# Kernel tuning notes

Hardware: AMD Instinct MI355X
Metric: run time of the kernel (lower is better)

## Reference

```python
import jax, jax.numpy as jnp
import numpy as np

B, N, T, CIN, HID, EMB, K = 32, 256, 13, 2, 64, 10, 2


def setup_inputs() -> dict:
    key = jax.random.key(0)
    ks = jax.random.split(key, 24)
    r = lambda i, shape, s=1.0: jax.random.normal(ks[i], shape, jnp.float32) * s
    return {
        "times": jnp.arange(T, dtype=jnp.float32),
        # natural cubic spline coefficients: (B, N, T-1, CIN)
        "coeff_a": r(0, (B, N, T - 1, CIN)),
        "coeff_b": r(1, (B, N, T - 1, CIN), 0.1),
        "coeff_two_c": r(2, (B, N, T - 1, CIN), 0.1),
        "coeff_three_d": r(3, (B, N, T - 1, CIN), 0.1),
        # initial_h / initial_z linear layers (input -> hidden)
        "W_h": r(4, (CIN, HID), 0.5), "b_h": r(5, (HID,), 0.1),
        "W_z": r(6, (CIN, HID), 0.5), "b_z": r(7, (HID,), 0.1),
        # func_f (FinalTanh_f): linear_in, one hidden linear, linear_out -> hidden*input
        "Wf_in": r(8, (HID, HID), 0.1), "bf_in": r(9, (HID,), 0.05),
        "Wf_hid": r(10, (HID, HID), 0.1), "bf_hid": r(11, (HID,), 0.05),
        "Wf_out": r(12, (HID, HID * CIN), 0.1), "bf_out": r(13, (HID * CIN,), 0.05),
        # func_g (VectorField_g, g_type='agc')
        "Wg_in": r(14, (HID, HID), 0.1), "bg_in": r(15, (HID,), 0.05),
        "Eg": r(16, (N, EMB)),
        "W_pool": r(17, (EMB, K, HID, HID), 0.1),
        "b_pool": r(18, (EMB, HID), 0.1),
        "Wg_out": r(19, (HID, HID * CIN), 0.1), "bg_out": r(20, (HID * CIN,), 0.05),
    }


def reference(times, coeff_a, coeff_b, coeff_two_c, coeff_three_d,
              W_h, b_h, W_z, b_z,
              Wf_in, bf_in, Wf_hid, bf_hid, Wf_out, bf_out,
              Wg_in, bg_in, Eg, W_pool, b_pool, Wg_out, bg_out):
    maxidx = coeff_b.shape[-2] - 1

    def dX_dt(t):  # NaturalCubicSpline.derivative
        idx = jnp.clip(jnp.searchsorted(times, t, side='right') - 1, 0, maxidx)
        frac = t - times[idx]
        b = coeff_b[..., idx, :]
        c = coeff_two_c[..., idx, :]
        d = coeff_three_d[..., idx, :]
        return b + (c + d * frac) * frac  # (B, N, CIN)

    # adaptive graph conv (agc) static pieces, cheb_k = 2
    A = jax.nn.softmax(jax.nn.relu(Eg @ Eg.T), axis=1)          # (N, N)
    supports = jnp.stack([jnp.eye(N, dtype=A.dtype), A])        # (K, N, N)
    Wn = jnp.einsum('nd,dkio->nkio', Eg, W_pool)                # (N, K, HID, HID)
    bn = Eg @ b_pool                                            # (N, HID)

    def func_f(h):  # FinalTanh_f: MLP -> (B, N, HID, CIN) field
        x = jax.nn.relu(h @ Wf_in + bf_in)
        x = jax.nn.relu(x @ Wf_hid + bf_hid)
        x = (x @ Wf_out + bf_out).reshape(*x.shape[:-1], HID, CIN)
        return jnp.tanh(x)

    def func_g(z):  # VectorField_g with agc
        x = jax.nn.relu(z @ Wg_in + bg_in)                       # (B, N, HID)
        x_g = jnp.einsum('knm,bmc->bnkc', supports, x)           # (B, N, K, HID)
        x = jnp.einsum('bnki,nkio->bno', x_g, Wn) + bn           # (B, N, HID)
        x = (x @ Wg_out + bg_out).reshape(*x.shape[:-1], HID, CIN)
        return jnp.tanh(x)

    def vf(t, h, z):  # VectorField_g_dev of cdeint_gde_dev
        dX = dX_dt(t)                                            # (B, N, CIN)
        f = func_f(h)
        g = func_g(z)
        dh = jnp.einsum('bnhi,bni->bnh', f, dX)
        dz = jnp.einsum('bnhi,bni->bnh', g * f, dX)
        return dh, dz

    # spline.evaluate(times[0]) == coeff_a[..., 0, :] (frac = 0)
    x0 = coeff_a[..., 0, :]
    h0 = x0 @ W_h + b_h
    z0 = x0 @ W_z + b_z

    third = jnp.float32(1.0 / 3.0)

    def step(carry, ts):  # torchdiffeq 'rk4' (3/8 rule), one step per interval
        h, z = carry
        t0, t1 = ts
        dt = t1 - t0
        k1h, k1z = vf(t0, h, z)
        k2h, k2z = vf(t0 + dt * third, h + dt * third * k1h, z + dt * third * k1z)
        k3h, k3z = vf(t0 + dt * 2 * third, h + dt * (k2h - third * k1h), z + dt * (k2z - third * k1z))
        k4h, k4z = vf(t1, h + dt * (k1h - k2h + k3h), z + dt * (k1z - k2z + k3z))
        h = h + dt * 0.125 * (k1h + 3.0 * (k2h + k3h) + k4h)
        z = z + dt * 0.125 * (k1z + 3.0 * (k2z + k3z) + k4z)
        return (h, z), z

    ts = jnp.stack([times[:-1], times[1:]], axis=1)              # (T-1, 2)
    (_, _), z_seq = jax.lax.scan(step, (h0, z0), ts)
    z_t = jnp.concatenate([z0[None], z_seq], axis=0)             # (T, B, N, HID)
    return jnp.transpose(z_t, (1, 2, 0, 3))                      # (B, N, T, HID)
```

## Files before the change

kernel.cpp:

```cpp
#include <hip/hip_runtime.h>

typedef unsigned short ushort_t;
typedef unsigned int uint_t;
typedef float f4v __attribute__((ext_vector_type(4)));

#define CW_OFF  0
#define A_OFF   524288
#define BN_OFF  786432
#define WN_OFF  851968
#define XB_OFF  5046272
#define H_OFF   7143424
#define Z_OFF   9240576
#define K1H_OFF 11337728
#define K1Z_OFF 13434880
#define K2H_OFF 15532032
#define K2Z_OFF 17629184
#define UH_OFF  19726336

#define F_X0     0
#define F_WH     16384
#define F_BH     16512
#define F_WZ     16576
#define F_BZ     16704
#define F_WFIN   16768
#define F_BFIN   20864
#define F_WFHID  20928
#define F_BFHID  25024
#define F_WFOUT  25088
#define F_BFOUT  33280
#define F_WGIN   33408
#define F_BGIN   37504
#define F_WGOUT  37568
#define F_BGOUT  45760
#define F_EG     45888
#define F_WPOOL  48448
#define F_BPOOL  130368

__device__ __forceinline__ float bfl(uint_t u){ union{uint_t i; float f;} c; c.i = u<<16; return c.f; }
__device__ __forceinline__ float bfh(uint_t u){ union{uint_t i; float f;} c; c.i = u & 0xffff0000u; return c.f; }
__device__ __forceinline__ float bf1(ushort_t u){ union{uint_t i; float f;} c; c.i = ((uint_t)u)<<16; return c.f; }
__device__ __forceinline__ uint_t f2bf(float x){
  uint_t u = __float_as_uint(x);
  uint_t r = u + 0x7fffu + ((u >> 16) & 1u);
  return r >> 16;
}
__device__ __forceinline__ float fast_tanh(float x){
  float e = __expf(2.0f*x);
  return 1.0f - 2.0f/(e+1.0f);
}
__device__ __forceinline__ bool inputs_are_f32(const void* times){
  return ((const uint_t*)times)[0] != 0x3F800000u;
}
__device__ __forceinline__ void ntst4(float* p, float a, float b, float c, float d){
  f4v v; v[0]=a; v[1]=b; v[2]=c; v[3]=d;
  __builtin_nontemporal_store(v, (f4v*)p);
}

__device__ __forceinline__ void dotf_4(const float* act, const float* W, int o0, float acc[4]) {
  const float4* a4 = (const float4*)act;
  #pragma unroll
  for (int i4 = 0; i4 < 16; ++i4) {
    float4 av4 = a4[i4];
    float av[4] = {av4.x, av4.y, av4.z, av4.w};
    #pragma unroll
    for (int ii = 0; ii < 4; ++ii) {
      float4 w = *(const float4*)(W + (i4*4+ii)*64 + o0);
      acc[0] += av[ii]*w.x; acc[1] += av[ii]*w.y;
      acc[2] += av[ii]*w.z; acc[3] += av[ii]*w.w;
    }
  }
}

__device__ __forceinline__ void dotf_8(const float* act, const float* W, int co0, float acc[8]) {
  const float4* a4 = (const float4*)act;
  #pragma unroll
  for (int i4 = 0; i4 < 16; ++i4) {
    float4 av4 = a4[i4];
    float av[4] = {av4.x, av4.y, av4.z, av4.w};
    #pragma unroll
    for (int ii = 0; ii < 4; ++ii) {
      const float* wp = W + (i4*4+ii)*128 + co0;
      float4 w0 = *(const float4*)(wp);
      float4 w1 = *(const float4*)(wp + 4);
      float a = av[ii];
      acc[0] += a*w0.x; acc[1] += a*w0.y; acc[2] += a*w0.z; acc[3] += a*w0.w;
      acc[4] += a*w1.x; acc[5] += a*w1.y; acc[6] += a*w1.z; acc[7] += a*w1.w;
    }
  }
}

__device__ __forceinline__ void cvt_copy(float* dst, const void* src, int cnt, bool f32in){
  if (f32in) {
    const float* s = (const float*)src;
    for (int i = threadIdx.x; i < cnt; i += 256) dst[i] = s[i];
  } else {
    const ushort_t* s = (const ushort_t*)src;
    for (int i = threadIdx.x; i < cnt; i += 256) dst[i] = bf1(s[i]);
  }
}

__global__ __launch_bounds__(256) void k_conv(
    const void* times, const void* ca,
    const void* W_h, const void* b_h, const void* W_z, const void* b_z,
    const void* Wf_in, const void* bf_in, const void* Wf_hid, const void* bf_hid,
    const void* Wf_out, const void* bf_out, const void* Wg_in, const void* bg_in,
    const void* Wg_out, const void* bg_out, const void* Eg, const void* W_pool,
    const void* b_pool, char* __restrict__ wsb)
{
  const bool f32in = inputs_are_f32(times);
  float* F = (float*)(wsb + CW_OFF);
  const int bid = blockIdx.x;
  if (bid < 4) {
    const int base = bid * 4096;
    if (f32in) {
      const float* s = (const float*)ca;
      for (int i = threadIdx.x; i < 4096; i += 256) {
        int g = base + i;
        F[F_X0 + g] = s[(g >> 1)*24 + (g & 1)];
      }
    } else {
      const ushort_t* s = (const ushort_t*)ca;
      for (int i = threadIdx.x; i < 4096; i += 256) {
        int g = base + i;
        F[F_X0 + g] = bf1(s[(g >> 1)*24 + (g & 1)]);
      }
    }
    return;
  }
  if (bid < 20) {
    const int off = (bid - 4) * 5120;
    const void* srcp = f32in ? (const void*)((const float*)W_pool + off)
                             : (const void*)((const ushort_t*)W_pool + off);
    cvt_copy(F + F_WPOOL + off, srcp, 5120, f32in);
    return;
  }
  const void* src = nullptr; int dst = 0, cnt = 0;
  switch (bid) {
    case 20: src = W_h;    dst = F_WH;    cnt = 128;  break;
    case 21: src = b_h;    dst = F_BH;    cnt = 64;   break;
    case 22: src = W_z;    dst = F_WZ;    cnt = 128;  break;
    case 23: src = b_z;    dst = F_BZ;    cnt = 64;   break;
    case 24: src = Wf_in;  dst = F_WFIN;  cnt = 4096; break;
    case 25: src = bf_in;  dst = F_BFIN;  cnt = 64;   break;
    case 26: src = Wf_hid; dst = F_WFHID; cnt = 4096; break;
    case 27: src = bf_hid; dst = F_BFHID; cnt = 64;   break;
    case 28: src = Wf_out; dst = F_WFOUT; cnt = 8192; break;
    case 29: src = bf_out; dst = F_BFOUT; cnt = 128;  break;
    case 30: src = Wg_in;  dst = F_WGIN;  cnt = 4096; break;
    case 31: src = bg_in;  dst = F_BGIN;  cnt = 64;   break;
    case 32: src = Wg_out; dst = F_WGOUT; cnt = 8192; break;
    case 33: src = bg_out; dst = F_BGOUT; cnt = 128;  break;
    case 34: src = Eg;     dst = F_EG;    cnt = 2560; break;
    default: src = b_pool; dst = F_BPOOL; cnt = 640;  break;
  }
  cvt_copy(F + dst, src, cnt, f32in);
}

__global__ __launch_bounds__(256) void k_A(char* __restrict__ wsb) {
  const float* F = (const float*)(wsb + CW_OFF);
  float* Aw = (float*)(wsb + A_OFF);
  float* bn = (float*)(wsb + BN_OFF);
  const int nrow = blockIdx.x;
  const int m = threadIdx.x;
  float eg_n[10];
  #pragma unroll
  for (int d = 0; d < 10; ++d) eg_n[d] = F[F_EG + nrow*10 + d];
  float dot = 0.f;
  #pragma unroll
  for (int d = 0; d < 10; ++d) dot += eg_n[d] * F[F_EG + m*10 + d];
  float v = fmaxf(dot, 0.f);
  __shared__ float red[256];
  red[m] = v; __syncthreads();
  for (int off = 128; off > 0; off >>= 1) {
    if (m < off) red[m] = fmaxf(red[m], red[m+off]);
    __syncthreads();
  }
  float vmax = red[0]; __syncthreads();
  float e = __expf(v - vmax);
  red[m] = e; __syncthreads();
  for (int off = 128; off > 0; off >>= 1) {
    if (m < off) red[m] += red[m+off];
    __syncthreads();
  }
  float ssum = red[0];
  Aw[nrow*256 + m] = e / ssum;
  if (m < 64) {
    float acc = 0.f;
    #pragma unroll
    for (int d = 0; d < 10; ++d) acc += eg_n[d] * F[F_BPOOL + d*64 + m];
    bn[nrow*64 + m] = acc;
  }
}

__global__ __launch_bounds__(256) void k_Wn(char* __restrict__ wsb) {
  const float* F = (const float*)(wsb + CW_OFF);
  ushort_t* Wn = (ushort_t*)(wsb + WN_OFF);
  int idx = blockIdx.x*256 + threadIdx.x;
  int o = idx & 63;
  int i = (idx >> 6) & 63;
  int k = (idx >> 12) & 1;
  int n = idx >> 13;
  float acc = 0.f;
  #pragma unroll
  for (int d = 0; d < 10; ++d)
    acc += F[F_EG + n*10 + d] * F[F_WPOOL + ((d*2 + k)*64 + i)*64 + o];
  Wn[idx] = (ushort_t)f2bf(acc);
}

__global__ __launch_bounds__(512) void k_init2(char* __restrict__ wsb, float* __restrict__ out) {
  const float* F = (const float*)(wsb + CW_OFF);
  float* H = (float*)(wsb + H_OFF);
  float* Z = (float*)(wsb + Z_OFF);
  ushort_t* X0 = (ushort_t*)(wsb + XB_OFF);

  const int tid = threadIdx.x;
  const int lr  = tid >> 4;
  const int o0  = (tid & 15) * 4;
  const int row = blockIdx.x * 32 + lr;

  __shared__ __align__(16) float sIn[32][68];

  float a0 = F[F_X0 + row*2 + 0];
  float a1 = F[F_X0 + row*2 + 1];
  float h[4], z[4];
  #pragma unroll
  for (int j = 0; j < 4; ++j) {
    h[j] = a0*F[F_WH + o0+j] + a1*F[F_WH + 64+o0+j] + F[F_BH + o0+j];
    z[j] = a0*F[F_WZ + o0+j] + a1*F[F_WZ + 64+o0+j] + F[F_BZ + o0+j];
  }
  *(float4*)(H + row*64 + o0) = make_float4(h[0],h[1],h[2],h[3]);
  *(float4*)(Z + row*64 + o0) = make_float4(z[0],z[1],z[2],z[3]);
  ntst4(out + (row*13)*64 + o0, z[0],z[1],z[2],z[3]);

  *(float4*)&sIn[lr][o0] = make_float4(z[0],z[1],z[2],z[3]);
  __syncthreads();
  float xr[4];
  { float4 bv = *(const float4*)(F + F_BGIN + o0);
    xr[0]=bv.x; xr[1]=bv.y; xr[2]=bv.z; xr[3]=bv.w; }
  dotf_4(&sIn[lr][0], F + F_WGIN, o0, xr);
  #pragma unroll
  for (int j=0;j<4;++j) xr[j] = fmaxf(xr[j], 0.f);
  { uint2 pk;
    pk.x = f2bf(xr[0]) | (f2bf(xr[1]) << 16);
    pk.y = f2bf(xr[2]) | (f2bf(xr[3]) << 16);
    *(uint2*)(X0 + row*64 + o0) = pk; }
}

__global__ __launch_bounds__(512) void k_stage(
    const void* __restrict__ times,
    const void* __restrict__ cbv, const void* __restrict__ ccv, const void* __restrict__ cdv,
    char* __restrict__ wsb, float* __restrict__ out, int vfc)
{
  const float* F  = (const float*)(wsb + CW_OFF);
  const float* Aw = (const float*)(wsb + A_OFF);
  const float* bn = (const float*)(wsb + BN_OFF);
  const ushort_t* Wn = (const ushort_t*)(wsb + WN_OFF);
  ushort_t* XB = (ushort_t*)(wsb + XB_OFF);
  float* H   = (float*)(wsb + H_OFF);
  float* Z   = (float*)(wsb + Z_OFF);
  float* K1h = (float*)(wsb + K1H_OFF);
  float* K1z = (float*)(wsb + K1Z_OFF);
  float* K2h = (float*)(wsb + K2H_OFF);
  float* K2z = (float*)(wsb + K2Z_OFF);
  float* UH  = (float*)(wsb + UH_OFF);
  const bool f32in = inputs_are_f32(times);

  const int s  = vfc >> 2;
  const int st = vfc & 3;
  const ushort_t* Xc = XB + (vfc & 1) * 524288;
  ushort_t*       Xn = XB + ((vfc + 1) & 1) * 524288;

  const int tid = threadIdx.x;
  const int lr  = tid >> 4;
  const int o0  = (tid & 15) * 4;
  const int co0 = o0 * 2;
  const int bb  = blockIdx.x >> 3;
  const int nr  = blockIdx.x & 7;
  const int n   = nr * 32 + lr;
  const int row = bb * 256 + n;

  __shared__ __align__(16) float sIn[32][68];
  __shared__ __align__(16) float sT [32][68];
  __shared__ __align__(16) float sX [32][68];
  __shared__ __align__(16) float xs [128][68];

  { uint2 w = *(const uint2*)(Xc + row*64 + o0);
    *(float4*)&sX[lr][o0] = make_float4(bfl(w.x), bfh(w.x), bfl(w.y), bfh(w.y)); }

  float y[4] = {0.f,0.f,0.f,0.f};
  const float* Arow = Aw + n*256;
  #pragma unroll 1
  for (int half = 0; half < 2; ++half) {
    __syncthreads();
    #pragma unroll
    for (int q = tid; q < 2048; q += 512) {
      int r = q >> 4, c4 = q & 15;
      uint2 w = *(const uint2*)(Xc + (bb*256 + half*128 + r)*64 + c4*4);
      *(float4*)&xs[r][c4*4] = make_float4(bfl(w.x), bfh(w.x), bfl(w.y), bfh(w.y));
    }
    __syncthreads();
    #pragma unroll 4
    for (int m4 = 0; m4 < 32; ++m4) {
      float4 av = *(const float4*)(Arow + half*128 + m4*4);
      float am[4] = {av.x, av.y, av.z, av.w};
      #pragma unroll
      for (int mm = 0; mm < 4; ++mm) {
        float4 xv = *(const float4*)&xs[m4*4+mm][o0];
        y[0] += am[mm]*xv.x; y[1] += am[mm]*xv.y;
        y[2] += am[mm]*xv.z; y[3] += am[mm]*xv.w;
      }
    }
  }

  __syncthreads();
  *(float4*)&sT[lr][o0] = make_float4(y[0],y[1],y[2],y[3]);
  __syncthreads();
  float og[4];
  { float4 bv = *(const float4*)(bn + n*64 + o0); og[0]=bv.x; og[1]=bv.y; og[2]=bv.z; og[3]=bv.w; }
  const ushort_t* W0 = Wn + n*8192;
  #pragma unroll
  for (int i4 = 0; i4 < 16; ++i4) {
    float4 xa = *(const float4*)&sX[lr][i4*4];
    float4 ya = *(const float4*)&sT[lr][i4*4];
    float xav[4]={xa.x,xa.y,xa.z,xa.w};
    float yav[4]={ya.x,ya.y,ya.z,ya.w};
    #pragma unroll
    for (int ii = 0; ii < 4; ++ii) {
      int i = i4*4 + ii;
      uint2 w0 = *(const uint2*)(W0 + i*64 + o0);
      uint2 w1 = *(const uint2*)(W0 + 4096 + i*64 + o0);
      og[0] += xav[ii]*bfl(w0.x) + yav[ii]*bfl(w1.x);
      og[1] += xav[ii]*bfh(w0.x) + yav[ii]*bfh(w1.x);
      og[2] += xav[ii]*bfl(w0.y) + yav[ii]*bfl(w1.y);
      og[3] += xav[ii]*bfh(w0.y) + yav[ii]*bfh(w1.y);
    }
  }
  *(float4*)&sIn[lr][o0] = make_float4(og[0],og[1],og[2],og[3]);
  __syncthreads();
  float go[8];
  { float4 b0 = *(const float4*)(F + F_BGOUT + co0);
    float4 b1 = *(const float4*)(F + F_BGOUT + co0 + 4);
    go[0]=b0.x; go[1]=b0.y; go[2]=b0.z; go[3]=b0.w;
    go[4]=b1.x; go[5]=b1.y; go[6]=b1.z; go[7]=b1.w; }
  dotf_8(&sIn[lr][0], F + F_WGOUT, co0, go);
  float g0[4], g1[4];
  #pragma unroll
  for (int j=0;j<4;++j){ g0[j]=fast_tanh(go[2*j]); g1[j]=fast_tanh(go[2*j+1]); }

  __syncthreads();
  { const float* UHsrc = (st == 0) ? H : UH;
    float4 uv = *(const float4*)(UHsrc + row*64 + o0);
    *(float4*)&sIn[lr][o0] = uv; }
  __syncthreads();
  float a1v[4];
  { float4 bv = *(const float4*)(F + F_BFIN + o0);
    a1v[0]=bv.x; a1v[1]=bv.y; a1v[2]=bv.z; a1v[3]=bv.w; }
  dotf_4(&sIn[lr][0], F + F_WFIN, o0, a1v);
  #pragma unroll
  for (int j=0;j<4;++j) a1v[j] = fmaxf(a1v[j], 0.f);
  *(float4*)&sT[lr][o0] = make_float4(a1v[0],a1v[1],a1v[2],a1v[3]);
  __syncthreads();
  float a2v[4];
  { float4 bv = *(const float4*)(F + F_BFHID + o0);
    a2v[0]=bv.x; a2v[1]=bv.y; a2v[2]=bv.z; a2v[3]=bv.w; }
  dotf_4(&sT[lr][0], F + F_WFHID, o0, a2v);
  #pragma unroll
  for (int j=0;j<4;++j) a2v[j] = fmaxf(a2v[j], 0.f);
  *(float4*)&sIn[lr][o0] = make_float4(a2v[0],a2v[1],a2v[2],a2v[3]);
  __syncthreads();
  float fo[8];
  { float4 b0 = *(const float4*)(F + F_BFOUT + co0);
    float4 b1 = *(const float4*)(F + F_BFOUT + co0 + 4);
    fo[0]=b0.x; fo[1]=b0.y; fo[2]=b0.z; fo[3]=b0.w;
    fo[4]=b1.x; fo[5]=b1.y; fo[6]=b1.z; fo[7]=b1.w; }
  dotf_8(&sIn[lr][0], F + F_WFOUT, co0, fo);
  float f0[4], f1[4];
  #pragma unroll
  for (int j=0;j<4;++j){ f0[j]=fast_tanh(fo[2*j]); f1[j]=fast_tanh(fo[2*j+1]); }

  int sidx; float frac;
  if (st == 0)      { sidx = s; frac = 0.f; }
  else if (st == 1) { sidx = s; frac = 0.33333334f; }
  else if (st == 2) { sidx = s; frac = 0.66666669f; }
  else              { sidx = (s < 11) ? s+1 : 11; frac = (s < 11) ? 0.f : 1.f; }
  float dX0, dX1;
  if (f32in) {
    float2 vb = *(const float2*)((const float*)cbv + (row*12 + sidx)*2);
    float2 vc = *(const float2*)((const float*)ccv + (row*12 + sidx)*2);
    float2 vd = *(const float2*)((const float*)cdv + (row*12 + sidx)*2);
    dX0 = vb.x + (vc.x + vd.x*frac)*frac;
    dX1 = vb.y + (vc.y + vd.y*frac)*frac;
  } else {
    uint_t vb = *(const uint_t*)((const ushort_t*)cbv + (row*12 + sidx)*2);
    uint_t vc = *(const uint_t*)((const ushort_t*)ccv + (row*12 + sidx)*2);
    uint_t vd = *(const uint_t*)((const ushort_t*)cdv + (row*12 + sidx)*2);
    dX0 = bfl(vb) + (bfl(vc) + bfl(vd)*frac)*frac;
    dX1 = bfh(vb) + (bfh(vc) + bfh(vd)*frac)*frac;
  }

  float dh[4], dz[4];
  #pragma unroll
  for (int j=0;j<4;++j){
    dh[j] = f0[j]*dX0 + f1[j]*dX1;
    dz[j] = g0[j]*f0[j]*dX0 + g1[j]*f1[j]*dX1;
  }

  float uh_n[4], uz_n[4];
  float4 hv = *(const float4*)(H + row*64 + o0);
  float4 zv = *(const float4*)(Z + row*64 + o0);
  float h[4] = {hv.x,hv.y,hv.z,hv.w};
  float z[4] = {zv.x,zv.y,zv.z,zv.w};

  if (st == 0) {
    *(float4*)(K1h + row*64 + o0) = make_float4(dh[0],dh[1],dh[2],dh[3]);
    *(float4*)(K1z + row*64 + o0) = make_float4(dz[0],dz[1],dz[2],dz[3]);
    #pragma unroll
    for (int j=0;j<4;++j){ uh_n[j]=h[j]+dh[j]*(1.f/3.f); uz_n[j]=z[j]+dz[j]*(1.f/3.f); }
  } else if (st == 1) {
    float4 k1hv = *(const float4*)(K1h + row*64 + o0);
    float4 k1zv = *(const float4*)(K1z + row*64 + o0);
    float k1hl[4]={k1hv.x,k1hv.y,k1hv.z,k1hv.w};
    float k1zl[4]={k1zv.x,k1zv.y,k1zv.z,k1zv.w};
    float Qh[4],Qz[4],Ph[4],Pz[4];
    #pragma unroll
    for (int j=0;j<4;++j){
      Qh[j]=k1hl[j]+3.f*dh[j]; Qz[j]=k1zl[j]+3.f*dz[j];
      Ph[j]=k1hl[j]-dh[j];     Pz[j]=k1zl[j]-dz[j];
      uh_n[j]=h[j]+dh[j]-k1hl[j]*(1.f/3.f);
      uz_n[j]=z[j]+dz[j]-k1zl[j]*(1.f/3.f);
    }
    *(float4*)(K1h + row*64 + o0) = make_float4(Qh[0],Qh[1],Qh[2],Qh[3]);
    *(float4*)(K1z + row*64 + o0) = make_float4(Qz[0],Qz[1],Qz[2],Qz[3]);
    *(float4*)(K2h + row*64 + o0) = make_float4(Ph[0],Ph[1],Ph[2],Ph[3]);
    *(float4*)(K2z + row*64 + o0) = make_float4(Pz[0],Pz[1],Pz[2],Pz[3]);
  } else if (st == 2) {
    float4 Qhv = *(const float4*)(K1h + row*64 + o0);
    float4 Qzv = *(const float4*)(K1z + row*64 + o0);
    float4 Phv = *(const float4*)(K2h + row*64 + o0);
    float4 Pzv = *(const float4*)(K2z + row*64 + o0);
    float Qh[4]={Qhv.x,Qhv.y,Qhv.z,Qhv.w}, Qz[4]={Qzv.x,Qzv.y,Qzv.z,Qzv.w};
    float Ph[4]={Phv.x,Phv.y,Phv.z,Phv.w}, Pz[4]={Pzv.x,Pzv.y,Pzv.z,Pzv.w};
    float Ah[4],Az[4];
    #pragma unroll
    for (int j=0;j<4;++j){
      Ah[j]=Qh[j]+3.f*dh[j]; Az[j]=Qz[j]+3.f*dz[j];
      uh_n[j]=h[j]+Ph[j]+dh[j];
      uz_n[j]=z[j]+Pz[j]+dz[j];
    }
    *(float4*)(K1h + row*64 + o0) = make_float4(Ah[0],Ah[1],Ah[2],Ah[3]);
    *(float4*)(K1z + row*64 + o0) = make_float4(Az[0],Az[1],Az[2],Az[3]);
  } else {
    float4 Ahv = *(const float4*)(K1h + row*64 + o0);
    float4 Azv = *(const float4*)(K1z + row*64 + o0);
    #pragma unroll
    for (int j=0;j<4;++j){
      float hn = h[j] + 0.125f*(((const float*)&Ahv)[j] + dh[j]);
      float zn = z[j] + 0.125f*(((const float*)&Azv)[j] + dz[j]);
      uh_n[j]=hn; uz_n[j]=zn;
    }
    *(float4*)(H + row*64 + o0) = make_float4(uh_n[0],uh_n[1],uh_n[2],uh_n[3]);
    *(float4*)(Z + row*64 + o0) = make_float4(uz_n[0],uz_n[1],uz_n[2],uz_n[3]);
    ntst4(out + (row*13 + s + 1)*64 + o0, uz_n[0],uz_n[1],uz_n[2],uz_n[3]);
  }

  if (vfc < 47) {
    *(float4*)(UH + row*64 + o0) = make_float4(uh_n[0],uh_n[1],uh_n[2],uh_n[3]);
    __syncthreads();
    *(float4*)&sIn[lr][o0] = make_float4(uz_n[0],uz_n[1],uz_n[2],uz_n[3]);
    __syncthreads();
    float xr[4];
    { float4 bv = *(const float4*)(F + F_BGIN + o0);
      xr[0]=bv.x; xr[1]=bv.y; xr[2]=bv.z; xr[3]=bv.w; }
    dotf_4(&sIn[lr][0], F + F_WGIN, o0, xr);
    #pragma unroll
    for (int j=0;j<4;++j) xr[j] = fmaxf(xr[j], 0.f);
    uint2 pk;
    pk.x = f2bf(xr[0]) | (f2bf(xr[1]) << 16);
    pk.y = f2bf(xr[2]) | (f2bf(xr[3]) << 16);
    *(uint2*)(Xn + row*64 + o0) = pk;
  }
}

extern "C" void kernel_launch(void* const* d_in, const int* in_sizes, int n_in,
                              void* d_out, int out_size, void* d_ws, size_t ws_size,
                              hipStream_t stream) {
  const void* times   = d_in[0];
  const void* coeff_a = d_in[1];
  const void* coeff_b = d_in[2];
  const void* coeff_c = d_in[3];
  const void* coeff_d = d_in[4];
  const void* W_h    = d_in[5];
  const void* b_h    = d_in[6];
  const void* W_z    = d_in[7];
  const void* b_z    = d_in[8];
  const void* Wf_in  = d_in[9];
  const void* bf_in  = d_in[10];
  const void* Wf_hid = d_in[11];
  const void* bf_hid = d_in[12];
  const void* Wf_out = d_in[13];
  const void* bf_out = d_in[14];
  const void* Wg_in  = d_in[15];
  const void* bg_in  = d_in[16];
  const void* Eg     = d_in[17];
  const void* W_pool = d_in[18];
  const void* b_pool = d_in[19];
  const void* Wg_out = d_in[20];
  const void* bg_out = d_in[21];

  char* wsb = (char*)d_ws;
  float* out = (float*)d_out;

  hipLaunchKernelGGL(k_conv, dim3(36), dim3(256), 0, stream,
                     times, coeff_a, W_h, b_h, W_z, b_z,
                     Wf_in, bf_in, Wf_hid, bf_hid, Wf_out, bf_out,
                     Wg_in, bg_in, Wg_out, bg_out, Eg, W_pool, b_pool, wsb);
  hipLaunchKernelGGL(k_A,    dim3(256),  dim3(256), 0, stream, wsb);
  hipLaunchKernelGGL(k_Wn,   dim3(8192), dim3(256), 0, stream, wsb);
  hipLaunchKernelGGL(k_init2, dim3(256), dim3(512), 0, stream, wsb, out);
  for (int vfc = 0; vfc < 48; ++vfc) {
    hipLaunchKernelGGL(k_stage, dim3(256), dim3(512), 0, stream,
                       times, coeff_b, coeff_c, coeff_d, wsb, out, vfc);
  }
}
```

Baseline: 5.173 ms.

## Interleave f-path MLP layers with graph aggregation halves to cut barriers

Restructures the per-stage vector-field kernel so the f-network's first two layers are computed between and alongside the two halves of the adjacency aggregation. Shared-memory buffers are reused and an extra sUH tile is added, which reduces the number of __syncthreads barriers per stage and lets independent work fill the wait around them. The gate output projection moves later and the tanh is fused into the dh/dz loop. This costs more shared memory, about 8.7KB extra, which may lower occupancy.

```diff
diff --git a/kernel.cpp b/kernel.cpp
--- a/kernel.cpp
+++ b/kernel.cpp
@@ -282,39 +282,74 @@
   __shared__ __align__(16) float sIn[32][68];
   __shared__ __align__(16) float sT [32][68];
   __shared__ __align__(16) float sX [32][68];
+  __shared__ __align__(16) float sUH[32][68];
   __shared__ __align__(16) float xs [128][68];
 
   { uint2 w = *(const uint2*)(Xc + row*64 + o0);
     *(float4*)&sX[lr][o0] = make_float4(bfl(w.x), bfh(w.x), bfl(w.y), bfh(w.y)); }
+  { const float* UHsrc = (st == 0) ? H : UH;
+    *(float4*)&sUH[lr][o0] = *(const float4*)(UHsrc + row*64 + o0); }
+  #pragma unroll
+  for (int q = tid; q < 2048; q += 512) {
+    int r = q >> 4, c4 = q & 15;
+    uint2 w = *(const uint2*)(Xc + (bb*256 + r)*64 + c4*4);
+    *(float4*)&xs[r][c4*4] = make_float4(bfl(w.x), bfh(w.x), bfl(w.y), bfh(w.y));
+  }
+  __syncthreads();
 
   float y[4] = {0.f,0.f,0.f,0.f};
   const float* Arow = Aw + n*256;
-  #pragma unroll 1
-  for (int half = 0; half < 2; ++half) {
-    __syncthreads();
-    #pragma unroll
-    for (int q = tid; q < 2048; q += 512) {
-      int r = q >> 4, c4 = q & 15;
-      uint2 w = *(const uint2*)(Xc + (bb*256 + half*128 + r)*64 + c4*4);
-      *(float4*)&xs[r][c4*4] = make_float4(bfl(w.x), bfh(w.x), bfl(w.y), bfh(w.y));
-    }
-    __syncthreads();
-    #pragma unroll 4
-    for (int m4 = 0; m4 < 32; ++m4) {
-      float4 av = *(const float4*)(Arow + half*128 + m4*4);
-      float am[4] = {av.x, av.y, av.z, av.w};
-      #pragma unroll
-      for (int mm = 0; mm < 4; ++mm) {
-        float4 xv = *(const float4*)&xs[m4*4+mm][o0];
-        y[0] += am[mm]*xv.x; y[1] += am[mm]*xv.y;
-        y[2] += am[mm]*xv.z; y[3] += am[mm]*xv.w;
-      }
-    }
-  }
-
-  __syncthreads();
-  *(float4*)&sT[lr][o0] = make_float4(y[0],y[1],y[2],y[3]);
-  __syncthreads();
+  #pragma unroll 4
+  for (int m4 = 0; m4 < 32; ++m4) {
+    float4 av = *(const float4*)(Arow + m4*4);
+    float am[4] = {av.x, av.y, av.z, av.w};
+    #pragma unroll
+    for (int mm = 0; mm < 4; ++mm) {
+      float4 xv = *(const float4*)&xs[m4*4+mm][o0];
+      y[0] += am[mm]*xv.x; y[1] += am[mm]*xv.y;
+      y[2] += am[mm]*xv.z; y[3] += am[mm]*xv.w;
+    }
+  }
+  float a1v[4];
+  { float4 bv = *(const float4*)(F + F_BFIN + o0);
+    a1v[0]=bv.x; a1v[1]=bv.y; a1v[2]=bv.z; a1v[3]=bv.w; }
+  dotf_4(&sUH[lr][0], F + F_WFIN, o0, a1v);
+  #pragma unroll
+  for (int j=0;j<4;++j) a1v[j] = fmaxf(a1v[j], 0.f);
+  __syncthreads();
+
+  #pragma unroll
+  for (int q = tid; q < 2048; q += 512) {
+    int r = q >> 4, c4 = q & 15;
+    uint2 w = *(const uint2*)(Xc + (bb*256 + 128 + r)*64 + c4*4);
+    *(float4*)&xs[r][c4*4] = make_float4(bfl(w.x), bfh(w.x), bfl(w.y), bfh(w.y));
+  }
+  *(float4*)&sT[lr][o0] = make_float4(a1v[0],a1v[1],a1v[2],a1v[3]);
+  __syncthreads();
+
+  #pragma unroll 4
+  for (int m4 = 0; m4 < 32; ++m4) {
+    float4 av = *(const float4*)(Arow + 128 + m4*4);
+    float am[4] = {av.x, av.y, av.z, av.w};
+    #pragma unroll
+    for (int mm = 0; mm < 4; ++mm) {
+      float4 xv = *(const float4*)&xs[m4*4+mm][o0];
+      y[0] += am[mm]*xv.x; y[1] += am[mm]*xv.y;
+      y[2] += am[mm]*xv.z; y[3] += am[mm]*xv.w;
+    }
+  }
+  float a2v[4];
+  { float4 bv = *(const float4*)(F + F_BFHID + o0);
+    a2v[0]=bv.x; a2v[1]=bv.y; a2v[2]=bv.z; a2v[3]=bv.w; }
+  dotf_4(&sT[lr][0], F + F_WFHID, o0, a2v);
+  #pragma unroll
+  for (int j=0;j<4;++j) a2v[j] = fmaxf(a2v[j], 0.f);
+  __syncthreads();
+
+  *(float4*)&sT [lr][o0] = make_float4(y[0],y[1],y[2],y[3]);
+  *(float4*)&sIn[lr][o0] = make_float4(a2v[0],a2v[1],a2v[2],a2v[3]);
+  __syncthreads();
+
   float og[4];
   { float4 bv = *(const float4*)(bn + n*64 + o0); og[0]=bv.x; og[1]=bv.y; og[2]=bv.z; og[3]=bv.w; }
   const ushort_t* W0 = Wn + n*8192;
@@ -335,39 +370,6 @@
       og[3] += xav[ii]*bfh(w0.y) + yav[ii]*bfh(w1.y);
     }
   }
-  *(float4*)&sIn[lr][o0] = make_float4(og[0],og[1],og[2],og[3]);
-  __syncthreads();
-  float go[8];
-  { float4 b0 = *(const float4*)(F + F_BGOUT + co0);
-    float4 b1 = *(const float4*)(F + F_BGOUT + co0 + 4);
-    go[0]=b0.x; go[1]=b0.y; go[2]=b0.z; go[3]=b0.w;
-    go[4]=b1.x; go[5]=b1.y; go[6]=b1.z; go[7]=b1.w; }
-  dotf_8(&sIn[lr][0], F + F_WGOUT, co0, go);
-  float g0[4], g1[4];
-  #pragma unroll
-  for (int j=0;j<4;++j){ g0[j]=fast_tanh(go[2*j]); g1[j]=fast_tanh(go[2*j+1]); }
-
-  __syncthreads();
-  { const float* UHsrc = (st == 0) ? H : UH;
-    float4 uv = *(const float4*)(UHsrc + row*64 + o0);
-    *(float4*)&sIn[lr][o0] = uv; }
-  __syncthreads();
-  float a1v[4];
-  { float4 bv = *(const float4*)(F + F_BFIN + o0);
-    a1v[0]=bv.x; a1v[1]=bv.y; a1v[2]=bv.z; a1v[3]=bv.w; }
-  dotf_4(&sIn[lr][0], F + F_WFIN, o0, a1v);
-  #pragma unroll
-  for (int j=0;j<4;++j) a1v[j] = fmaxf(a1v[j], 0.f);
-  *(float4*)&sT[lr][o0] = make_float4(a1v[0],a1v[1],a1v[2],a1v[3]);
-  __syncthreads();
-  float a2v[4];
-  { float4 bv = *(const float4*)(F + F_BFHID + o0);
-    a2v[0]=bv.x; a2v[1]=bv.y; a2v[2]=bv.z; a2v[3]=bv.w; }
-  dotf_4(&sT[lr][0], F + F_WFHID, o0, a2v);
-  #pragma unroll
-  for (int j=0;j<4;++j) a2v[j] = fmaxf(a2v[j], 0.f);
-  *(float4*)&sIn[lr][o0] = make_float4(a2v[0],a2v[1],a2v[2],a2v[3]);
-  __syncthreads();
   float fo[8];
   { float4 b0 = *(const float4*)(F + F_BFOUT + co0);
     float4 b1 = *(const float4*)(F + F_BFOUT + co0 + 4);
@@ -397,12 +399,23 @@
     dX0 = bfl(vb) + (bfl(vc) + bfl(vd)*frac)*frac;
     dX1 = bfh(vb) + (bfh(vc) + bfh(vd)*frac)*frac;
   }
-
+  *(float4*)&sUH[lr][o0] = make_float4(og[0],og[1],og[2],og[3]);
+  __syncthreads();
+
+  float go[8];
+  { float4 b0 = *(const float4*)(F + F_BGOUT + co0);
+    float4 b1 = *(const float4*)(F + F_BGOUT + co0 + 4);
+    go[0]=b0.x; go[1]=b0.y; go[2]=b0.z; go[3]=b0.w;
+    go[4]=b1.x; go[5]=b1.y; go[6]=b1.z; go[7]=b1.w; }
+  dotf_8(&sUH[lr][0], F + F_WGOUT, co0, go);
   float dh[4], dz[4];
   #pragma unroll
   for (int j=0;j<4;++j){
-    dh[j] = f0[j]*dX0 + f1[j]*dX1;
-    dz[j] = g0[j]*f0[j]*dX0 + g1[j]*f1[j]*dX1;
+    float g0 = fast_tanh(go[2*j]);
+    float g1 = fast_tanh(go[2*j+1]);
+    float p0 = f0[j]*dX0, p1 = f1[j]*dX1;
+    dh[j] = p0 + p1;
+    dz[j] = g0*p0 + g1*p1;
   }
 
   float uh_n[4], uz_n[4];
@@ -465,13 +478,13 @@
 
   if (vfc < 47) {
     *(float4*)(UH + row*64 + o0) = make_float4(uh_n[0],uh_n[1],uh_n[2],uh_n[3]);
+    *(float4*)&sT[lr][o0] = make_float4(uz_n[0],uz_n[1],uz_n[2],uz_n[3]);
     __syncthreads();
-    *(float4*)&sIn[lr][o0] = make_float4(uz_n[0],uz_n[1],uz_n[2],uz_n[3]);
-    __syncthreads();
+
     float xr[4];
     { float4 bv = *(const float4*)(F + F_BGIN + o0);
       xr[0]=bv.x; xr[1]=bv.y; xr[2]=bv.z; xr[3]=bv.w; }
-    dotf_4(&sIn[lr][0], F + F_WGIN, o0, xr);
+    dotf_4(&sT[lr][0], F + F_WGIN, o0, xr);
     #pragma unroll
     for (int j=0;j<4;++j) xr[j] = fmaxf(xr[j], 0.f);
     uint2 pk;
```

New measurement: 13.85 ms. 168% more time.
